# Performance work log

Hardware: AMD Instinct MI355X
Metric: run time of the kernel (lower is better)

The kernel has to match this reference:

```python
import jax, jax.numpy as jnp
import numpy as np

# Mamba2 hyperparams (from config['block'][0])
D_MODEL = 512
D_STATE = 64
D_CONV = 4
EXPAND = 2
HEADDIM = 64
D_INNER = EXPAND * D_MODEL          # 1024
NHEADS = D_INNER // HEADDIM         # 16
CONV_DIM = D_INNER + 2 * D_STATE    # 1152 (x, B, C share the depthwise conv)
D_IN_PROJ = 2 * D_INNER + 2 * D_STATE + NHEADS  # z | xBC | dt
EPS = 1e-5
BATCH, SEQLEN = 2, 4096


def setup_inputs() -> dict:
    key = jax.random.key(0)
    ks = jax.random.split(key, 10)
    x = jax.random.normal(ks[0], (BATCH, SEQLEN, D_MODEL), dtype=jnp.float32)
    W_in = jax.random.normal(ks[1], (D_MODEL, D_IN_PROJ), dtype=jnp.float32) * 0.02
    conv_w = jax.random.normal(ks[2], (CONV_DIM, 1, D_CONV), dtype=jnp.float32) * 0.2
    conv_b = jax.random.normal(ks[3], (CONV_DIM,), dtype=jnp.float32) * 0.02
    dt_bias = jax.random.uniform(ks[4], (NHEADS,), minval=-4.0, maxval=-1.0, dtype=jnp.float32)
    A_log = jnp.log(jax.random.uniform(ks[5], (NHEADS,), minval=1.0, maxval=16.0, dtype=jnp.float32))
    D = jax.random.normal(ks[6], (NHEADS,), dtype=jnp.float32) * 0.5 + 1.0
    norm_weight = jnp.ones((D_INNER,), dtype=jnp.float32)
    W_out = jax.random.normal(ks[7], (D_INNER, D_MODEL), dtype=jnp.float32) * 0.02
    return {"x": x, "W_in": W_in, "conv_w": conv_w, "conv_b": conv_b,
            "dt_bias": dt_bias, "A_log": A_log, "D": D,
            "norm_weight": norm_weight, "W_out": W_out}


def _mamba2_forward(x, W_in, conv_w, conv_b, dt_bias, A_log, D, norm_weight, W_out):
    b, l, _ = x.shape
    zxbcdt = x @ W_in                                      # (b, l, D_IN_PROJ)
    z = zxbcdt[..., :D_INNER]                              # gate branch
    xBC = zxbcdt[..., D_INNER:D_INNER + CONV_DIM]
    dt = zxbcdt[..., D_INNER + CONV_DIM:]                  # (b, l, h)

    # depthwise causal conv1d over sequence, then SiLU
    xBC_ncw = jnp.transpose(xBC, (0, 2, 1))                # (b, c, l)
    xBC_ncw = jax.lax.conv_general_dilated(
        xBC_ncw, conv_w, window_strides=(1,), padding=[(D_CONV - 1, 0)],
        dimension_numbers=("NCW", "OIW", "NCW"), feature_group_count=CONV_DIM)
    xBC_ncw = xBC_ncw + conv_b[None, :, None]
    xBC = jax.nn.silu(jnp.transpose(xBC_ncw, (0, 2, 1)))   # (b, l, c)

    x_ssm = xBC[..., :D_INNER].reshape(b, l, NHEADS, HEADDIM)  # (b,l,h,p)
    B = xBC[..., D_INNER:D_INNER + D_STATE]                    # (b,l,n)
    C = xBC[..., D_INNER + D_STATE:]                           # (b,l,n)

    dt = jax.nn.softplus(dt + dt_bias)                     # (b,l,h)
    A = -jnp.exp(A_log)                                    # (h,)
    dA = jnp.exp(dt * A)                                   # (b,l,h) discrete decay

    # selective scan: state s has shape (b, h, p, n)
    def step(s, inp):
        dA_t, dt_t, x_t, B_t, C_t = inp                    # (b,h),(b,h),(b,h,p),(b,n),(b,n)
        dBx = (dt_t[..., None] * x_t)[..., None] * B_t[:, None, None, :]
        s = s * dA_t[..., None, None] + dBx
        y_t = jnp.einsum("bhpn,bn->bhp", s, C_t)
        return s, y_t

    s0 = jnp.zeros((b, NHEADS, HEADDIM, D_STATE), dtype=x.dtype)
    xs = (jnp.moveaxis(dA, 1, 0), jnp.moveaxis(dt, 1, 0),
          jnp.moveaxis(x_ssm, 1, 0), jnp.moveaxis(B, 1, 0), jnp.moveaxis(C, 1, 0))
    _, ys = jax.lax.scan(step, s0, xs)                     # ys: (l,b,h,p)
    y = jnp.moveaxis(ys, 0, 1)                             # (b,l,h,p)

    y = y + D[None, None, :, None] * x_ssm                 # skip term
    y = y.reshape(b, l, D_INNER)

    # gated RMSNorm (norm after gating, mamba2 default)
    y = y * jax.nn.silu(z)
    var = jnp.mean(jnp.square(y), axis=-1, keepdims=True)
    y = y * jax.lax.rsqrt(var + EPS) * norm_weight

    return y @ W_out                                       # (b, l, d_model)


def reference(x, W_in, conv_w, conv_b, dt_bias, A_log, D, norm_weight, W_out):
    return _mamba2_forward(x, W_in, conv_w, conv_b, dt_bias, A_log, D, norm_weight, W_out)
```

## Files before the change

### kernel.cpp

```cpp
#include <hip/hip_runtime.h>
#include <hip/hip_bf16.h>

#define BATCH   2
#define SEQ     4096
#define DMODEL  512
#define DINNER  1024
#define DSTATE  64
#define NHEADS  16
#define HEADDIM 64
#define CONVDIM 1152
#define NPROJ   2192
#define NPROJ_PAD 2304
#define MROWS   (BATCH*SEQ)
#define QCH     64
#define NCHUNK  (SEQ/QCH)

typedef short bf16x8 __attribute__((ext_vector_type(8)));
typedef float f32x4  __attribute__((ext_vector_type(4)));
using bf16 = __hip_bfloat16;
typedef unsigned short ushort_t;
typedef unsigned int   uint_t;

__device__ __forceinline__ float sigmoidf_(float x) { return 1.f / (1.f + __expf(-x)); }
__device__ __forceinline__ float bf2f(ushort_t u) { return __uint_as_float((uint_t)u << 16); }
__device__ __forceinline__ ushort_t f2bfu(float f) {
    bf16 h = __float2bfloat16(f);
    return *(ushort_t*)&h;
}
__device__ __forceinline__ void bf8_to_f(const ushort_t* __restrict__ p, float* __restrict__ f) {
    uint4 u = *(const uint4*)p;
    f[0] = __uint_as_float((u.x & 0xFFFFu) << 16);
    f[1] = __uint_as_float(u.x & 0xFFFF0000u);
    f[2] = __uint_as_float((u.y & 0xFFFFu) << 16);
    f[3] = __uint_as_float(u.y & 0xFFFF0000u);
    f[4] = __uint_as_float((u.z & 0xFFFFu) << 16);
    f[5] = __uint_as_float(u.z & 0xFFFF0000u);
    f[6] = __uint_as_float((u.w & 0xFFFFu) << 16);
    f[7] = __uint_as_float(u.w & 0xFFFF0000u);
}
__device__ __forceinline__ uint4 f8_to_bf(const float* __restrict__ f) {
    union { ushort_t s[8]; uint4 u; } r;
#pragma unroll
    for (int i = 0; i < 8; i++) r.s[i] = f2bfu(f[i]);
    return r.u;
}

__device__ __forceinline__ void gload_lds16(const ushort_t* g, ushort_t* l)
{
    __builtin_amdgcn_global_load_lds(
        (const __attribute__((address_space(1))) void*)g,
        (__attribute__((address_space(3)))       void*)l,
        16, 0, 0);
}

__global__ void cast_f32_bf16_k(const float* __restrict__ in, ushort_t* __restrict__ out, int n8)
{
    int i = blockIdx.x * 256 + threadIdx.x;
    if (i >= n8) return;
    float f[8];
    *(float4*)(f + 0) = ((const float4*)in)[i * 2 + 0];
    *(float4*)(f + 4) = ((const float4*)in)[i * 2 + 1];
    ((uint4*)out)[i] = f8_to_bf(f);
}

__global__ void transpose_f32_bf16_k(const float* __restrict__ in, ushort_t* __restrict__ out,
                                     int R, int C, int Cpad)
{
    __shared__ __align__(16) ushort_t tile[32][33];
    int c0 = blockIdx.x * 32, r0 = blockIdx.y * 32;
    int tx = threadIdx.x, ty = threadIdx.y;
#pragma unroll
    for (int i = 0; i < 32; i += 8) {
        int r = r0 + ty + i, c = c0 + tx;
        tile[ty + i][tx] = (r < R && c < C) ? f2bfu(in[(size_t)r * C + c]) : (ushort_t)0;
    }
    __syncthreads();
#pragma unroll
    for (int i = 0; i < 32; i += 8) {
        int orow = c0 + ty + i, ocol = r0 + tx;
        if (orow < Cpad && ocol < R) out[(size_t)orow * R + ocol] = tile[tx][ty + i];
    }
}

__global__ void bcconv_k(const ushort_t* __restrict__ xpbc, const float* __restrict__ cw,
                         const float* __restrict__ cb, ushort_t* __restrict__ bcc)
{
    int idx = blockIdx.x * 256 + threadIdx.x;
    int row = idx >> 4, c8 = (idx & 15) * 8;
    int l = row & (SEQ - 1);
    float acc[8];
#pragma unroll
    for (int i = 0; i < 8; i++) acc[i] = cb[1024 + c8 + i];
#pragma unroll
    for (int j = 0; j < 4; j++) {
        int ll = l - 3 + j;
        if (ll >= 0) {
            float v[8];
            bf8_to_f(xpbc + (size_t)(row - 3 + j) * 128 + c8, v);
#pragma unroll
            for (int i = 0; i < 8; i++) acc[i] += cw[(1024 + c8 + i) * 4 + j] * v[i];
        }
    }
#pragma unroll
    for (int i = 0; i < 8; i++) { float v = acc[i]; acc[i] = v * sigmoidf_(v); }
    *(uint4*)(bcc + (size_t)row * 128 + c8) = f8_to_bf(acc);
}

template<int MODE>
__global__ __launch_bounds__(256, 3)
void gemm_k(const ushort_t* __restrict__ A, const ushort_t* __restrict__ Bt,
            ushort_t* __restrict__ zbuf, ushort_t* __restrict__ xpx,
            ushort_t* __restrict__ xpbc, float* __restrict__ dtv,
            float* __restrict__ dalog, const float* __restrict__ dt_b,
            const float* __restrict__ A_log, float* __restrict__ outf,
            int M, int N, int K)
{
    constexpr int SC = 132;
    __shared__ __align__(16) ushort_t smem[128 * SC];
    ushort_t* As = smem;
    ushort_t* Bs = smem + 128 * 64;
    ushort_t* Cs = smem;

    const int tid  = threadIdx.x;
    const int wave = tid >> 6, lane = tid & 63;
    const int quad = lane >> 4, l16 = lane & 15;
    const int wm = (wave >> 1) * 64, wn = (wave & 1) * 64;
    const int m0 = blockIdx.y * 128, n0 = blockIdx.x * 128;

    const int srow = lane >> 3;
    const int scol = (lane & 7) * 8;
    const ushort_t* ag = A  + (size_t)(m0 + wave * 32 + srow) * K + scol;
    const ushort_t* bg = Bt + (size_t)(n0 + wave * 32 + srow) * K + scol;
    ushort_t* al = As + wave * 32 * 64;
    ushort_t* bl = Bs + wave * 32 * 64;

    f32x4 acc[4][4];
#pragma unroll
    for (int i = 0; i < 4; i++)
#pragma unroll
        for (int j = 0; j < 4; j++) acc[i][j] = (f32x4){0.f, 0.f, 0.f, 0.f};

    for (int k0 = 0; k0 < K; k0 += 64) {
        __syncthreads();
#pragma unroll
        for (int j = 0; j < 4; j++) {
            gload_lds16(ag + (size_t)(j * 8) * K + k0, al + j * 8 * 64);
            gload_lds16(bg + (size_t)(j * 8) * K + k0, bl + j * 8 * 64);
        }
        __syncthreads();
#pragma unroll
        for (int kk = 0; kk < 64; kk += 32) {
            bf16x8 af[4], bfr[4];
#pragma unroll
            for (int i = 0; i < 4; i++)
                af[i] = *(const bf16x8*)(&As[(wm + i * 16 + l16) * 64 + kk + quad * 8]);
#pragma unroll
            for (int j = 0; j < 4; j++)
                bfr[j] = *(const bf16x8*)(&Bs[(wn + j * 16 + l16) * 64 + kk + quad * 8]);
#pragma unroll
            for (int i = 0; i < 4; i++)
#pragma unroll
                for (int j = 0; j < 4; j++)
                    acc[i][j] = __builtin_amdgcn_mfma_f32_16x16x32_bf16(af[i], bfr[j], acc[i][j], 0, 0, 0);
        }
    }
    if (MODE == 1) {
#pragma unroll
        for (int i = 0; i < 4; i++)
#pragma unroll
            for (int j = 0; j < 4; j++) {
                int col = n0 + wn + j * 16 + l16;
                int rowb = m0 + wm + i * 16 + quad * 4;
#pragma unroll
                for (int r = 0; r < 4; r++)
                    outf[(size_t)(rowb + r) * N + col] = acc[i][j][r];
            }
    } else if (n0 == 2176) {
#pragma unroll
        for (int i = 0; i < 4; i++)
#pragma unroll
            for (int j = 0; j < 4; j++) {
                int col = n0 + wn + j * 16 + l16;
                int rowb = m0 + wm + i * 16 + quad * 4;
                if (col < N) {
                    int hh = col - 2176;
#pragma unroll
                    for (int r = 0; r < 4; r++) {
                        float v = acc[i][j][r];
                        size_t g = (size_t)(rowb + r);
                        float raw = v + dt_b[hh];
                        float sp  = (raw > 20.f) ? raw : log1pf(__expf(raw));
                        dtv  [g * NHEADS + hh] = sp;
                        dalog[g * NHEADS + hh] = -__expf(A_log[hh]) * sp;
                    }
                }
            }
    } else {
        __syncthreads();
#pragma unroll
        for (int i = 0; i < 4; i++)
#pragma unroll
            for (int j = 0; j < 4; j++)
#pragma unroll
                for (int r = 0; r < 4; r++)
                    Cs[(wm + i * 16 + quad * 4 + r) * SC + wn + j * 16 + l16] = f2bfu(acc[i][j][r]);
        __syncthreads();
        ushort_t* dst; int ld, coff;
        if (n0 < 1024)      { dst = zbuf; ld = 1024; coff = n0; }
        else if (n0 < 2048) { dst = xpx;  ld = 1024; coff = n0 - 1024; }
        else                { dst = xpbc; ld = 128;  coff = 0; }
#pragma unroll
        for (int jj = 0; jj < 8; jj++) {
            int idx = jj * 256 + tid;
            int row = idx >> 4, cq = (idx & 15) * 8;
            uint4 v = *(const uint4*)&Cs[row * SC + cq];
            *(uint4*)&dst[(size_t)(m0 + row) * ld + coff + cq] = v;
        }
    }
}

__global__ __launch_bounds__(256, 2)
void chunk_state_k(const ushort_t* __restrict__ xpx, const ushort_t* __restrict__ bcc,
                   const float* __restrict__ dtv, const float* __restrict__ dalog,
                   const float* __restrict__ cw, const float* __restrict__ cb,
                   ushort_t* __restrict__ statesT, float* __restrict__ cdecay)
{
    const int c = blockIdx.x, h = blockIdx.y, b = blockIdx.z;
    __shared__ __align__(16) ushort_t xsT[64 * 72];
    __shared__ __align__(16) ushort_t BwT[64 * 72];
    __shared__ float wc[64];
    const int tid = threadIdx.x;
    const int ts = tid >> 2, q4 = (tid & 3) * 16;
    const int l = c * QCH + ts;
    if (tid < 64) {
        size_t gl = ((size_t)b * SEQ + c * QCH + tid) * NHEADS + h;
        float v = dalog[gl];
#pragma unroll
        for (int off = 1; off < 64; off <<= 1) {
            float u = __shfl_up(v, off, 64);
            if (tid >= off) v += u;
        }
        float tot = __shfl(v, 63, 64);
        wc[tid] = __expf(tot - v) * dtv[gl];
        if (tid == 63) cdecay[(c * BATCH + b) * NHEADS + h] = __expf(tot);
    }
    __syncthreads();
    {
        const int ch0 = h * HEADDIM + q4;
        float a16[16];
#pragma unroll
        for (int i = 0; i < 16; i++) a16[i] = cb[ch0 + i];
#pragma unroll
        for (int j = 0; j < 4; j++) {
            int ll = l - 3 + j;
            if (ll >= 0) {
                float xv[16];
                const ushort_t* rp = xpx + ((size_t)b * SEQ + ll) * 1024 + ch0;
                bf8_to_f(rp, xv); bf8_to_f(rp + 8, xv + 8);
#pragma unroll
                for (int i = 0; i < 16; i++) a16[i] += cw[(ch0 + i) * 4 + j] * xv[i];
            }
        }
#pragma unroll
        for (int i = 0; i < 16; i++) { float v = a16[i]; xsT[(q4 + i) * 72 + ts] = f2bfu(v * sigmoidf_(v)); }
    }
    {
        float bv[16];
        const ushort_t* rp = bcc + ((size_t)b * SEQ + l) * 128;
        bf8_to_f(rp + q4, bv); bf8_to_f(rp + q4 + 8, bv + 8);
        const float wt = wc[ts];
#pragma unroll
        for (int i = 0; i < 16; i++) BwT[(q4 + i) * 72 + ts] = f2bfu(bv[i] * wt);
    }
    __syncthreads();
    const int wave = tid >> 6, lane = tid & 63;
    const int quad = lane >> 4, l16 = lane & 15;
    f32x4 acc[4];
#pragma unroll
    for (int j = 0; j < 4; j++) acc[j] = (f32x4){0.f, 0.f, 0.f, 0.f};
#pragma unroll
    for (int kk = 0; kk < 64; kk += 32) {
        bf16x8 af = *(const bf16x8*)(&xsT[(wave * 16 + l16) * 72 + kk + quad * 8]);
#pragma unroll
        for (int j = 0; j < 4; j++) {
            bf16x8 bf_ = *(const bf16x8*)(&BwT[(j * 16 + l16) * 72 + kk + quad * 8]);
            acc[j] = __builtin_amdgcn_mfma_f32_16x16x32_bf16(af, bf_, acc[j], 0, 0, 0);
        }
    }
    ushort_t* base = statesT + ((size_t)(c * BATCH + b) * NHEADS + h) * (HEADDIM * DSTATE);
#pragma unroll
    for (int j = 0; j < 4; j++)
#pragma unroll
        for (int r = 0; r < 4; r++)
            base[(wave * 16 + quad * 4 + r) * 64 + j * 16 + l16] = f2bfu(acc[j][r]);
}

__global__ void scan_combine_k(ushort_t* __restrict__ states, const float* __restrict__ cdecay)
{
    const int blk = blockIdx.x;
    const int quarter = blk & 3;
    const int h = (blk >> 2) & 15;
    const int b = blk >> 6;
    const int tid = threadIdx.x;
    __shared__ float dec[64];
    if (tid < 64) dec[tid] = cdecay[(tid * BATCH + b) * NHEADS + h];
    __syncthreads();
    const size_t cstride = (size_t)BATCH * NHEADS * HEADDIM * DSTATE;
    ushort_t* base = states + ((size_t)b * NHEADS + h) * (HEADDIM * DSTATE) + quarter * 1024 + tid * 4;
    float sx = 0.f, sy = 0.f, sz = 0.f, sw = 0.f;
    uint2 pre[4];
#pragma unroll
    for (int j = 0; j < 4; j++) pre[j] = *(const uint2*)(base + j * cstride);
    for (int c = 0; c < NCHUNK; c++) {
        uint2 Sc = pre[c & 3];
        if (c + 4 < NCHUNK) pre[c & 3] = *(const uint2*)(base + (size_t)(c + 4) * cstride);
        float d = dec[c];
        uint2 o;
        o.x = (uint_t)f2bfu(sx) | ((uint_t)f2bfu(sy) << 16);
        o.y = (uint_t)f2bfu(sz) | ((uint_t)f2bfu(sw) << 16);
        *(uint2*)(base + (size_t)c * cstride) = o;
        sx = d * sx + __uint_as_float((Sc.x & 0xFFFFu) << 16);
        sy = d * sy + __uint_as_float(Sc.x & 0xFFFF0000u);
        sz = d * sz + __uint_as_float((Sc.y & 0xFFFFu) << 16);
        sw = d * sw + __uint_as_float(Sc.y & 0xFFFF0000u);
    }
}

__global__ __launch_bounds__(256, 2)
void chunk_y_k(const ushort_t* __restrict__ xpx, const ushort_t* __restrict__ bcc,
               ushort_t* zio,
               const float* __restrict__ dtv, const float* __restrict__ dalog,
               const ushort_t* __restrict__ statesT, const float* __restrict__ cw,
               const float* __restrict__ cb, const float* __restrict__ Dp)
{
    const int c = blockIdx.x, h = blockIdx.y, b = blockIdx.z;
    __shared__ __align__(16) ushort_t CLb [64 * 72];
    __shared__ __align__(16) ushort_t BLb [64 * 72];
    __shared__ __align__(16) ushort_t xsT [64 * 72];
    __shared__ __align__(16) ushort_t attL[64 * 72];
    __shared__ float cum[64], wdt[64];
    const int tid = threadIdx.x;
    const int ts = tid >> 2, q4 = (tid & 3) * 16;
    const int l = c * QCH + ts;
    const float Dh = Dp[h];
    {
        const int ch0 = h * HEADDIM + q4;
        float a16[16];
#pragma unroll
        for (int i = 0; i < 16; i++) a16[i] = cb[ch0 + i];
#pragma unroll
        for (int j = 0; j < 4; j++) {
            int ll = l - 3 + j;
            if (ll >= 0) {
                float xv[16];
                const ushort_t* rp = xpx + ((size_t)b * SEQ + ll) * 1024 + ch0;
                bf8_to_f(rp, xv); bf8_to_f(rp + 8, xv + 8);
#pragma unroll
                for (int i = 0; i < 16; i++) a16[i] += cw[(ch0 + i) * 4 + j] * xv[i];
            }
        }
#pragma unroll
        for (int i = 0; i < 16; i++) { float v = a16[i]; xsT[(q4 + i) * 72 + ts] = f2bfu(v * sigmoidf_(v)); }
    }
    {
        const ushort_t* rp = bcc + ((size_t)b * SEQ + l) * 128;
        *(uint4*)&BLb[ts * 72 + q4]     = *(const uint4*)(rp + q4);
        *(uint4*)&BLb[ts * 72 + q4 + 8] = *(const uint4*)(rp + q4 + 8);
        *(uint4*)&CLb[ts * 72 + q4]     = *(const uint4*)(rp + 64 + q4);
        *(uint4*)&CLb[ts * 72 + q4 + 8] = *(const uint4*)(rp + 64 + q4 + 8);
    }
    if (tid < 64) {
        size_t gl = ((size_t)b * SEQ + c * QCH + tid) * NHEADS + h;
        float v = dalog[gl];
#pragma unroll
        for (int off = 1; off < 64; off <<= 1) {
            float u = __shfl_up(v, off, 64);
            if (tid >= off) v += u;
        }
        cum[tid] = v;
        wdt[tid] = dtv[gl];
    }
    __syncthreads();
    const int wave = tid >> 6, lane = tid & 63;
    const int quad = lane >> 4, l16 = lane & 15;
    {
        f32x4 sacc[4];
#pragma unroll
        for (int j = 0; j < 4; j++) sacc[j] = (f32x4){0.f, 0.f, 0.f, 0.f};
#pragma unroll
        for (int kk = 0; kk < 64; kk += 32) {
            bf16x8 af = *(const bf16x8*)(&CLb[(wave * 16 + l16) * 72 + kk + quad * 8]);
#pragma unroll
            for (int j = 0; j < 4; j++) {
                bf16x8 bf_ = *(const bf16x8*)(&BLb[(j * 16 + l16) * 72 + kk + quad * 8]);
                sacc[j] = __builtin_amdgcn_mfma_f32_16x16x32_bf16(af, bf_, sacc[j], 0, 0, 0);
            }
        }
#pragma unroll
        for (int r = 0; r < 4; r++) {
            const int t = wave * 16 + quad * 4 + r;
            const float ct = cum[t];
#pragma unroll
            for (int j = 0; j < 4; j++) {
                const int s = j * 16 + l16;
                float a = (s <= t) ? sacc[j][r] * __expf(ct - cum[s]) * wdt[s] : 0.f;
                attL[t * 72 + s] = f2bfu(a);
            }
        }
    }
    __syncthreads();
    {
        f32x4 accY[4], accI[4];
#pragma unroll
        for (int j = 0; j < 4; j++) { accY[j] = (f32x4){0.f, 0.f, 0.f, 0.f}; accI[j] = (f32x4){0.f, 0.f, 0.f, 0.f}; }
        const ushort_t* spg = statesT + ((size_t)(c * BATCH + b) * NHEADS + h) * (HEADDIM * DSTATE);
#pragma unroll
        for (int kk = 0; kk < 64; kk += 32) {
            bf16x8 a2 = *(const bf16x8*)(&attL[(wave * 16 + l16) * 72 + kk + quad * 8]);
            bf16x8 a3 = *(const bf16x8*)(&CLb [(wave * 16 + l16) * 72 + kk + quad * 8]);
#pragma unroll
            for (int j = 0; j < 4; j++) {
                bf16x8 b2 = *(const bf16x8*)(&xsT[(j * 16 + l16) * 72 + kk + quad * 8]);
                accY[j] = __builtin_amdgcn_mfma_f32_16x16x32_bf16(a2, b2, accY[j], 0, 0, 0);
                bf16x8 b3 = *(const bf16x8*)(spg + (j * 16 + l16) * 64 + kk + quad * 8);
                accI[j] = __builtin_amdgcn_mfma_f32_16x16x32_bf16(a3, b3, accI[j], 0, 0, 0);
            }
        }
#pragma unroll
        for (int r = 0; r < 4; r++) {
            const int t = wave * 16 + quad * 4 + r;
            const float et = __expf(cum[t]);
#pragma unroll
            for (int j = 0; j < 4; j++) {
                const int p = j * 16 + l16;
                float xv = bf2f(xsT[p * 72 + t]);
                float y = accY[j][r] + et * accI[j][r] + Dh * xv;
                BLb[t * 72 + p] = f2bfu(y);
            }
        }
    }
    __syncthreads();
    {
        ushort_t* zrow = zio + ((size_t)b * SEQ + l) * DINNER + h * HEADDIM + q4;
        float zv[16], yv[16], o[16];
        bf8_to_f(zrow, zv); bf8_to_f(zrow + 8, zv + 8);
        bf8_to_f(&BLb[ts * 72 + q4], yv); bf8_to_f(&BLb[ts * 72 + q4 + 8], yv + 8);
#pragma unroll
        for (int j = 0; j < 16; j++) {
            float z = zv[j];
            o[j] = yv[j] * z * sigmoidf_(z);
        }
        *(uint4*)(zrow)     = f8_to_bf(o);
        *(uint4*)(zrow + 8) = f8_to_bf(o + 8);
    }
}

__global__ void rmsnorm_k(ushort_t* yio, const float* __restrict__ nw)
{
    const int row = blockIdx.x, tid = threadIdx.x;
    uint2 u = *(const uint2*)(yio + (size_t)row * DINNER + tid * 4);
    float v0 = __uint_as_float((u.x & 0xFFFFu) << 16);
    float v1 = __uint_as_float(u.x & 0xFFFF0000u);
    float v2 = __uint_as_float((u.y & 0xFFFFu) << 16);
    float v3 = __uint_as_float(u.y & 0xFFFF0000u);
    float ss = v0 * v0 + v1 * v1 + v2 * v2 + v3 * v3;
#pragma unroll
    for (int off = 32; off >= 1; off >>= 1) ss += __shfl_xor(ss, off, 64);
    __shared__ float part[4];
    const int wave = tid >> 6;
    if ((tid & 63) == 0) part[wave] = ss;
    __syncthreads();
    float tot = part[0] + part[1] + part[2] + part[3];
    float scale = rsqrtf(tot * (1.f / DINNER) + 1e-5f);
    uint2 o;
    o.x = (uint_t)f2bfu(v0 * scale * nw[tid * 4 + 0]) | ((uint_t)f2bfu(v1 * scale * nw[tid * 4 + 1]) << 16);
    o.y = (uint_t)f2bfu(v2 * scale * nw[tid * 4 + 2]) | ((uint_t)f2bfu(v3 * scale * nw[tid * 4 + 3]) << 16);
    *(uint2*)(yio + (size_t)row * DINNER + tid * 4) = o;
}

extern "C" void kernel_launch(void* const* d_in, const int* in_sizes, int n_in,
                              void* d_out, int out_size, void* d_ws, size_t ws_size,
                              hipStream_t stream)
{
    const float* x      = (const float*)d_in[0];
    const float* W_in   = (const float*)d_in[1];
    const float* conv_w = (const float*)d_in[2];
    const float* conv_b = (const float*)d_in[3];
    const float* dt_b   = (const float*)d_in[4];
    const float* A_log  = (const float*)d_in[5];
    const float* Dp     = (const float*)d_in[6];
    const float* nw     = (const float*)d_in[7];
    const float* W_out  = (const float*)d_in[8];
    float* out = (float*)d_out;

    char* w = (char*)d_ws;
    ushort_t* zbuf    = (ushort_t*)(w);
    ushort_t* xpx     = (ushort_t*)(w + 16777216);
    ushort_t* statesT = (ushort_t*)(w + 33554432);
    ushort_t* WoutT   = (ushort_t*)(w + 33554432);
    char* dscr = (char*)d_out;
    ushort_t* xpbc  = (ushort_t*)(dscr);
    float*    dtv   = (float*)(dscr + 2097152);
    float*    dalog = (float*)(dscr + 2621440);
    float*    cdec  = (float*)(dscr + 3145728);
    ushort_t* WinT  = (ushort_t*)(dscr + 4194304);
    ushort_t* bcc   = (ushort_t*)(dscr + 4194304);
    ushort_t* xb    = (ushort_t*)(dscr + 8388608);

    cast_f32_bf16_k<<<(MROWS * DMODEL / 8 + 255) / 256, 256, 0, stream>>>(x, xb, MROWS * DMODEL / 8);
    transpose_f32_bf16_k<<<dim3(NPROJ_PAD / 32, DMODEL / 32), dim3(32, 8), 0, stream>>>(W_in, WinT, DMODEL, NPROJ, NPROJ_PAD);
    gemm_k<0><<<dim3(NPROJ_PAD / 128, MROWS / 128), 256, 0, stream>>>(
        xb, WinT, zbuf, xpx, xpbc, dtv, dalog, dt_b, A_log, nullptr,
        MROWS, NPROJ, DMODEL);
    bcconv_k<<<MROWS * 16 / 256, 256, 0, stream>>>(xpbc, conv_w, conv_b, bcc);
    chunk_state_k<<<dim3(NCHUNK, NHEADS, BATCH), 256, 0, stream>>>(
        xpx, bcc, dtv, dalog, conv_w, conv_b, statesT, cdec);
    scan_combine_k<<<BATCH * NHEADS * 4, 256, 0, stream>>>(statesT, cdec);
    chunk_y_k<<<dim3(NCHUNK, NHEADS, BATCH), 256, 0, stream>>>(
        xpx, bcc, zbuf, dtv, dalog, statesT, conv_w, conv_b, Dp);
    rmsnorm_k<<<MROWS, 256, 0, stream>>>(zbuf, nw);
    transpose_f32_bf16_k<<<dim3(DMODEL / 32, DINNER / 32), dim3(32, 8), 0, stream>>>(W_out, WoutT, DINNER, DMODEL, DMODEL);
    gemm_k<1><<<dim3(DMODEL / 128, MROWS / 128), 256, 0, stream>>>(
        zbuf, WoutT, nullptr, nullptr, nullptr, nullptr, nullptr, nullptr,
        nullptr, out, MROWS, DMODEL, DINNER);
}
```

Before: 238.5 us.

## Fuse RMSNorm into output GEMM and fold norm weight into W_out

Removes the separate rmsnorm kernel. The norm weight is folded into the transposed W_out, and the per-row sum of squares is accumulated from A fragments inside the output GEMM, then applied as a scale in the epilogue. The output GEMM also moves to 64-wide N tiles for more blocks, and the chunk kernels get higher occupancy hints in their launch bounds. The trade-off is extra ALU work per K step in half the waves, and a small numerics difference because the bf16 unnormalized y now feeds the MFMA.

```diff
diff --git a/kernel.cpp b/kernel.cpp
--- a/kernel.cpp
+++ b/kernel.cpp
@@ -64,7 +64,7 @@
 }
 
 __global__ void transpose_f32_bf16_k(const float* __restrict__ in, ushort_t* __restrict__ out,
-                                     int R, int C, int Cpad)
+                                     int R, int C, int Cpad, const float* __restrict__ sv)
 {
     __shared__ __align__(16) ushort_t tile[32][33];
     int c0 = blockIdx.x * 32, r0 = blockIdx.y * 32;
@@ -72,7 +72,9 @@
 #pragma unroll
     for (int i = 0; i < 32; i += 8) {
         int r = r0 + ty + i, c = c0 + tx;
-        tile[ty + i][tx] = (r < R && c < C) ? f2bfu(in[(size_t)r * C + c]) : (ushort_t)0;
+        float v = (r < R && c < C) ? in[(size_t)r * C + c] : 0.f;
+        if (sv && r < R) v *= sv[r];
+        tile[ty + i][tx] = f2bfu(v);
     }
     __syncthreads();
 #pragma unroll
@@ -107,7 +109,7 @@
 }
 
 template<int MODE>
-__global__ __launch_bounds__(256, 3)
+__global__ __launch_bounds__(256, MODE == 1 ? 4 : 3)
 void gemm_k(const ushort_t* __restrict__ A, const ushort_t* __restrict__ Bt,
             ushort_t* __restrict__ zbuf, ushort_t* __restrict__ xpx,
             ushort_t* __restrict__ xpbc, float* __restrict__ dtv,
@@ -115,8 +117,11 @@
             const float* __restrict__ A_log, float* __restrict__ outf,
             int M, int N, int K)
 {
+    constexpr int TN = (MODE == 1) ? 64 : 128;
+    constexpr int NJ = TN / 32;
     constexpr int SC = 132;
-    __shared__ __align__(16) ushort_t smem[128 * SC];
+    constexpr int SMEM_ELTS = (MODE == 1) ? (128 * 64 + TN * 64) : (128 * SC);
+    __shared__ __align__(16) ushort_t smem[SMEM_ELTS];
     ushort_t* As = smem;
     ushort_t* Bs = smem + 128 * 64;
     ushort_t* Cs = smem;
@@ -124,62 +129,87 @@
     const int tid  = threadIdx.x;
     const int wave = tid >> 6, lane = tid & 63;
     const int quad = lane >> 4, l16 = lane & 15;
-    const int wm = (wave >> 1) * 64, wn = (wave & 1) * 64;
-    const int m0 = blockIdx.y * 128, n0 = blockIdx.x * 128;
+    const int wm = (wave >> 1) * 64, wn = (wave & 1) * (TN / 2);
+    const int m0 = blockIdx.y * 128, n0 = blockIdx.x * TN;
 
     const int srow = lane >> 3;
     const int scol = (lane & 7) * 8;
-    const ushort_t* ag = A  + (size_t)(m0 + wave * 32 + srow) * K + scol;
-    const ushort_t* bg = Bt + (size_t)(n0 + wave * 32 + srow) * K + scol;
+    const ushort_t* ag = A  + (size_t)(m0 + wave * 32       + srow) * K + scol;
+    const ushort_t* bg = Bt + (size_t)(n0 + wave * (TN / 4) + srow) * K + scol;
     ushort_t* al = As + wave * 32 * 64;
-    ushort_t* bl = Bs + wave * 32 * 64;
-
-    f32x4 acc[4][4];
+    ushort_t* bl = Bs + wave * (TN / 4) * 64;
+
+    f32x4 acc[4][NJ];
 #pragma unroll
     for (int i = 0; i < 4; i++)
 #pragma unroll
-        for (int j = 0; j < 4; j++) acc[i][j] = (f32x4){0.f, 0.f, 0.f, 0.f};
+        for (int j = 0; j < NJ; j++) acc[i][j] = (f32x4){0.f, 0.f, 0.f, 0.f};
+    float ssq4[4] = {0.f, 0.f, 0.f, 0.f};
 
     for (int k0 = 0; k0 < K; k0 += 64) {
         __syncthreads();
 #pragma unroll
-        for (int j = 0; j < 4; j++) {
+        for (int j = 0; j < 4; j++)
             gload_lds16(ag + (size_t)(j * 8) * K + k0, al + j * 8 * 64);
+#pragma unroll
+        for (int j = 0; j < NJ; j++)
             gload_lds16(bg + (size_t)(j * 8) * K + k0, bl + j * 8 * 64);
-        }
         __syncthreads();
 #pragma unroll
         for (int kk = 0; kk < 64; kk += 32) {
-            bf16x8 af[4], bfr[4];
+            bf16x8 af[4], bfr[NJ];
 #pragma unroll
             for (int i = 0; i < 4; i++)
                 af[i] = *(const bf16x8*)(&As[(wm + i * 16 + l16) * 64 + kk + quad * 8]);
 #pragma unroll
-            for (int j = 0; j < 4; j++)
+            for (int j = 0; j < NJ; j++)
                 bfr[j] = *(const bf16x8*)(&Bs[(wn + j * 16 + l16) * 64 + kk + quad * 8]);
 #pragma unroll
             for (int i = 0; i < 4; i++)
 #pragma unroll
-                for (int j = 0; j < 4; j++)
+                for (int j = 0; j < NJ; j++)
                     acc[i][j] = __builtin_amdgcn_mfma_f32_16x16x32_bf16(af[i], bfr[j], acc[i][j], 0, 0, 0);
+            if (MODE == 1 && (wave & 1) == 0) {
+#pragma unroll
+                for (int i = 0; i < 4; i++)
+#pragma unroll
+                    for (int e = 0; e < 8; e++) {
+                        float f = bf2f((ushort_t)af[i][e]);
+                        ssq4[i] += f * f;
+                    }
+            }
         }
     }
     if (MODE == 1) {
+        __syncthreads();
+        float* smemf = (float*)smem;
+        if ((wave & 1) == 0) {
+#pragma unroll
+            for (int i = 0; i < 4; i++) {
+                float s = ssq4[i];
+                s += __shfl_xor(s, 16, 64);
+                s += __shfl_xor(s, 32, 64);
+                if (quad == 0) smemf[wm + i * 16 + l16] = s;
+            }
+        }
+        __syncthreads();
 #pragma unroll
         for (int i = 0; i < 4; i++)
 #pragma unroll
-            for (int j = 0; j < 4; j++) {
-                int col = n0 + wn + j * 16 + l16;
-                int rowb = m0 + wm + i * 16 + quad * 4;
-#pragma unroll
-                for (int r = 0; r < 4; r++)
-                    outf[(size_t)(rowb + r) * N + col] = acc[i][j][r];
+            for (int j = 0; j < NJ; j++) {
+                int col  = n0 + wn + j * 16 + l16;
+                int rowl = wm + i * 16 + quad * 4;
+#pragma unroll
+                for (int r = 0; r < 4; r++) {
+                    float sc = rsqrtf(smemf[rowl + r] * (1.f / DINNER) + 1e-5f);
+                    outf[(size_t)(m0 + rowl + r) * N + col] = acc[i][j][r] * sc;
+                }
             }
     } else if (n0 == 2176) {
 #pragma unroll
         for (int i = 0; i < 4; i++)
 #pragma unroll
-            for (int j = 0; j < 4; j++) {
+            for (int j = 0; j < NJ; j++) {
                 int col = n0 + wn + j * 16 + l16;
                 int rowb = m0 + wm + i * 16 + quad * 4;
                 if (col < N) {
@@ -200,7 +230,7 @@
 #pragma unroll
         for (int i = 0; i < 4; i++)
 #pragma unroll
-            for (int j = 0; j < 4; j++)
+            for (int j = 0; j < NJ; j++)
 #pragma unroll
                 for (int r = 0; r < 4; r++)
                     Cs[(wm + i * 16 + quad * 4 + r) * SC + wn + j * 16 + l16] = f2bfu(acc[i][j][r]);
@@ -219,7 +249,7 @@
     }
 }
 
-__global__ __launch_bounds__(256, 2)
+__global__ __launch_bounds__(256, 3)
 void chunk_state_k(const ushort_t* __restrict__ xpx, const ushort_t* __restrict__ bcc,
                    const float* __restrict__ dtv, const float* __restrict__ dalog,
                    const float* __restrict__ cw, const float* __restrict__ cb,
@@ -326,7 +356,7 @@
     }
 }
 
-__global__ __launch_bounds__(256, 2)
+__global__ __launch_bounds__(256, 3)
 void chunk_y_k(const ushort_t* __restrict__ xpx, const ushort_t* __restrict__ bcc,
                ushort_t* zio,
                const float* __restrict__ dtv, const float* __restrict__ dalog,
@@ -453,29 +483,6 @@
         *(uint4*)(zrow)     = f8_to_bf(o);
         *(uint4*)(zrow + 8) = f8_to_bf(o + 8);
     }
-}
-
-__global__ void rmsnorm_k(ushort_t* yio, const float* __restrict__ nw)
-{
-    const int row = blockIdx.x, tid = threadIdx.x;
-    uint2 u = *(const uint2*)(yio + (size_t)row * DINNER + tid * 4);
-    float v0 = __uint_as_float((u.x & 0xFFFFu) << 16);
-    float v1 = __uint_as_float(u.x & 0xFFFF0000u);
-    float v2 = __uint_as_float((u.y & 0xFFFFu) << 16);
-    float v3 = __uint_as_float(u.y & 0xFFFF0000u);
-    float ss = v0 * v0 + v1 * v1 + v2 * v2 + v3 * v3;
-#pragma unroll
-    for (int off = 32; off >= 1; off >>= 1) ss += __shfl_xor(ss, off, 64);
-    __shared__ float part[4];
-    const int wave = tid >> 6;
-    if ((tid & 63) == 0) part[wave] = ss;
-    __syncthreads();
-    float tot = part[0] + part[1] + part[2] + part[3];
-    float scale = rsqrtf(tot * (1.f / DINNER) + 1e-5f);
-    uint2 o;
-    o.x = (uint_t)f2bfu(v0 * scale * nw[tid * 4 + 0]) | ((uint_t)f2bfu(v1 * scale * nw[tid * 4 + 1]) << 16);
-    o.y = (uint_t)f2bfu(v2 * scale * nw[tid * 4 + 2]) | ((uint_t)f2bfu(v3 * scale * nw[tid * 4 + 3]) << 16);
-    *(uint2*)(yio + (size_t)row * DINNER + tid * 4) = o;
 }
 
 extern "C" void kernel_launch(void* const* d_in, const int* in_sizes, int n_in,
@@ -508,7 +515,7 @@
     ushort_t* xb    = (ushort_t*)(dscr + 8388608);
 
     cast_f32_bf16_k<<<(MROWS * DMODEL / 8 + 255) / 256, 256, 0, stream>>>(x, xb, MROWS * DMODEL / 8);
-    transpose_f32_bf16_k<<<dim3(NPROJ_PAD / 32, DMODEL / 32), dim3(32, 8), 0, stream>>>(W_in, WinT, DMODEL, NPROJ, NPROJ_PAD);
+    transpose_f32_bf16_k<<<dim3(NPROJ_PAD / 32, DMODEL / 32), dim3(32, 8), 0, stream>>>(W_in, WinT, DMODEL, NPROJ, NPROJ_PAD, nullptr);
     gemm_k<0><<<dim3(NPROJ_PAD / 128, MROWS / 128), 256, 0, stream>>>(
         xb, WinT, zbuf, xpx, xpbc, dtv, dalog, dt_b, A_log, nullptr,
         MROWS, NPROJ, DMODEL);
@@ -518,9 +525,8 @@
     scan_combine_k<<<BATCH * NHEADS * 4, 256, 0, stream>>>(statesT, cdec);
     chunk_y_k<<<dim3(NCHUNK, NHEADS, BATCH), 256, 0, stream>>>(
         xpx, bcc, zbuf, dtv, dalog, statesT, conv_w, conv_b, Dp);
-    rmsnorm_k<<<MROWS, 256, 0, stream>>>(zbuf, nw);
-    transpose_f32_bf16_k<<<dim3(DMODEL / 32, DINNER / 32), dim3(32, 8), 0, stream>>>(W_out, WoutT, DINNER, DMODEL, DMODEL);
-    gemm_k<1><<<dim3(DMODEL / 128, MROWS / 128), 256, 0, stream>>>(
+    transpose_f32_bf16_k<<<dim3(DMODEL / 32, DINNER / 32), dim3(32, 8), 0, stream>>>(W_out, WoutT, DINNER, DMODEL, DMODEL, nw);
+    gemm_k<1><<<dim3(DMODEL / 64, MROWS / 128), 256, 0, stream>>>(
         zbuf, WoutT, nullptr, nullptr, nullptr, nullptr, nullptr, nullptr,
         nullptr, out, MROWS, DMODEL, DINNER);
 }
```

New measurement: 233.5 us. -2.1%, faster.
